# Kernel tuning notes

Measured on AMD Instinct MI355X. Metric: run time of the kernel, lower is better.

The kernel has to match this reference:

```python
import jax, jax.numpy as jnp
import numpy as np

DEPTH = 17                      # tree depth (root at level 0)
D_IN = 128                      # input embedding dim
H = 128                         # hidden dim
N = 2 ** (DEPTH + 1) - 1        # total nodes in complete binary tree, level-major order


def setup_inputs() -> dict:
    key = jax.random.key(0)
    ks = jax.random.split(key, 13)
    s = 0.05
    inp = {"x": jax.random.normal(ks[0], (N, D_IN), jnp.float32)}
    # nn.Linear params; W stored as (in, out) so y = x @ W + b
    gate_names = ["i", "f", "o", "u"]
    for g, k in zip(gate_names, range(1, 5)):
        k1, k2, k3 = jax.random.split(ks[k], 3)
        inp[f"W_{g}"] = jax.random.normal(k1, (D_IN, H), jnp.float32) * s
        inp[f"b_{g}"] = jax.random.normal(k2, (H,), jnp.float32) * s
        inp[f"U_{g}"] = jax.random.normal(k3, (H, H), jnp.float32) * s
    inp["depth"] = DEPTH
    return inp


def reference(x, W_i, b_i, U_i, W_f, b_f, U_f, W_o, b_o, U_o, W_u, b_u, U_u, depth):
    # Precompute input contributions for ALL nodes in one GEMM per gate.
    Xi = x @ W_i + b_i  # [N, H]
    Xf = x @ W_f + b_f
    Xo = x @ W_o + b_o
    Xu = x @ W_u + b_u

    def lvl(l):
        return 2 ** l - 1, 2 ** l  # (start offset, n nodes) at level l

    # Leaves (level = depth): no children -> h_tilde = 0, c = i*u
    s0, n0 = lvl(depth)
    i = jax.nn.sigmoid(Xi[s0:s0 + n0])
    o = jax.nn.sigmoid(Xo[s0:s0 + n0])
    u = jnp.tanh(Xu[s0:s0 + n0])
    c = i * u
    h = o * jnp.tanh(c)

    # Process levels bottom-up; every internal node has exactly 2 children
    for l in range(depth - 1, -1, -1):
        sl, nl = lvl(l)
        ch = h.reshape(nl, 2, H)   # child hidden states per parent
        cc = c.reshape(nl, 2, H)   # child cell states per parent
        h_tilde = ch.sum(axis=1)   # child-sum
        i = jax.nn.sigmoid(Xi[sl:sl + nl] + h_tilde @ U_i)
        o = jax.nn.sigmoid(Xo[sl:sl + nl] + h_tilde @ U_o)
        u = jnp.tanh(Xu[sl:sl + nl] + h_tilde @ U_u)
        # per-child forget gates: f_j = sigmoid(W_f x + U_f h_j)
        f = jax.nn.sigmoid(Xf[sl:sl + nl][:, None, :] + ch @ U_f)  # [nl, 2, H]
        c = i * u + (f * cc).sum(axis=1)
        h = o * jnp.tanh(c)

    # Root (hidden, cell) stacked as [2, H]
    return jnp.stack([h[0], c[0]])
```

## Files before the change

### kernel.cpp

```cpp
#include <hip/hip_runtime.h>
#include <hip/hip_bf16.h>


typedef __bf16 bf16_t;
typedef __bf16 bf16x8 __attribute__((ext_vector_type(8)));
typedef float  f32x4  __attribute__((ext_vector_type(4)));

#define MFMA16(a, b, c) __builtin_amdgcn_mfma_f32_16x16x32_bf16((a), (b), (c), 0, 0, 0)

__device__ __forceinline__ float rcp_(float x) { return __builtin_amdgcn_rcpf(x); }
__device__ __forceinline__ float sigm(float x) { return rcp_(1.0f + __expf(-x)); }
__device__ __forceinline__ float tanh_(float x) {
    float a = fabsf(x);
    float e = __expf(2.0f * a);
    float t = fmaf(-2.0f, rcp_(e + 1.0f), 1.0f);
    return copysignf(t, x);
}

__device__ __forceinline__ void cvt16(const float* __restrict__ src, bf16_t* __restrict__ dst)
{
    float tmp[16];
    *(float4*)&tmp[0]  = ((const float4*)src)[0];
    *(float4*)&tmp[4]  = ((const float4*)src)[1];
    *(float4*)&tmp[8]  = ((const float4*)src)[2];
    *(float4*)&tmp[12] = ((const float4*)src)[3];
    bf16_t b[16];
#pragma unroll
    for (int j = 0; j < 16; j++) b[j] = (bf16_t)tmp[j];
    *(bf16x8*)&dst[0] = *(bf16x8*)&b[0];
    *(bf16x8*)&dst[8] = *(bf16x8*)&b[8];
}

__device__ __forceinline__ void zero16(bf16_t* __restrict__ dst)
{
    bf16x8 z = (bf16x8)(bf16_t)0.f;
    *(bf16x8*)&dst[0] = z;
    *(bf16x8*)&dst[8] = z;
}

__global__ __launch_bounds__(256)
void k_prep(const float* __restrict__ Wi, const float* __restrict__ Wf,
            const float* __restrict__ Wo, const float* __restrict__ Wu,
            const float* __restrict__ Ui, const float* __restrict__ Uf,
            const float* __restrict__ Uo, const float* __restrict__ Uu,
            bf16_t* __restrict__ SW)
{
    int b = blockIdx.x;
    const float* src;
    switch (b) {
        case 0: src = Wi; break; case 1: src = Wf; break;
        case 2: src = Wo; break; case 3: src = Wu; break;
        case 4: src = Ui; break; case 5: src = Uf; break;
        case 6: src = Uo; break; default: src = Uu; break;
    }
    if (b < 4) {
        bf16_t* hi = SW + (size_t)b * 16384;
        for (int idx = threadIdx.x; idx < 16384; idx += 256) {
            int j = idx & 7, ln = (idx >> 3) & 63, kb = (idx >> 9) & 3, nt = idx >> 11;
            int k = kb * 32 + (ln >> 4) * 8 + j;
            int n = nt * 16 + (ln & 15);
            hi[idx] = (bf16_t)src[k * 128 + n];
        }
    } else {
        bf16_t* hi = SW + 65536 + (size_t)(b - 4) * 32768;
        bf16_t* lo = hi + 16384;
        for (int idx = threadIdx.x; idx < 16384; idx += 256) {
            int j = idx & 7, ln = (idx >> 3) & 63, kb = (idx >> 9) & 3, nt = idx >> 11;
            int k = kb * 32 + (ln >> 4) * 8 + j;
            int n = nt * 16 + (ln & 15);
            float w = src[k * 128 + n];
            bf16_t hh = (bf16_t)w;
            hi[idx] = hh;
            lo[idx] = (bf16_t)(w - (float)hh);
        }
    }
}

__device__ __forceinline__ void leaf64(
    const float* __restrict__ x, const bf16_t* __restrict__ SW,
    const float* __restrict__ bi, const float* __restrict__ bo,
    const float* __restrict__ bu,
    bf16_t (* __restrict__ XA)[136],
    bf16_t (* __restrict__ BH)[136], bf16_t (* __restrict__ BC)[136],
    int xRowBase, int tid)
{
    {
        int r = tid >> 3, cb = (tid & 7) * 16;
        cvt16(x + (size_t)(xRowBase + r - 1) * 128 + cb, &XA[r][cb]);
        cvt16(x + (size_t)(xRowBase + r + 31) * 128 + cb, &XA[r + 32][cb]);
    }
    __syncthreads();
    const int wave = tid >> 6, lane = tid & 63;
    const int quad = lane >> 4, lc = lane & 15;

    f32x4 aI[2][4], aO[2][4], aU[2][4];
#pragma unroll
    for (int nt = 0; nt < 2; nt++)
#pragma unroll
        for (int mt = 0; mt < 4; mt++) {
            aI[nt][mt] = (f32x4){0.f, 0.f, 0.f, 0.f};
            aO[nt][mt] = (f32x4){0.f, 0.f, 0.f, 0.f};
            aU[nt][mt] = (f32x4){0.f, 0.f, 0.f, 0.f};
        }
    for (int kb = 0; kb < 4; kb++) {
        const int k0 = kb * 32 + quad * 8;
        bf16x8 a0 = *(const bf16x8*)&XA[lc][k0];
        bf16x8 a1 = *(const bf16x8*)&XA[16 + lc][k0];
        bf16x8 a2 = *(const bf16x8*)&XA[32 + lc][k0];
        bf16x8 a3 = *(const bf16x8*)&XA[48 + lc][k0];
#pragma unroll
        for (int nt = 0; nt < 2; nt++) {
            const size_t boff = ((size_t)((2 * wave + nt) * 4 + kb) * 64 + lane) * 8;
            bf16x8 bWi = *(const bf16x8*)(SW + boff);
            bf16x8 bWo = *(const bf16x8*)(SW + 32768 + boff);
            bf16x8 bWu = *(const bf16x8*)(SW + 49152 + boff);
            aI[nt][0] = MFMA16(a0, bWi, aI[nt][0]);
            aI[nt][1] = MFMA16(a1, bWi, aI[nt][1]);
            aI[nt][2] = MFMA16(a2, bWi, aI[nt][2]);
            aI[nt][3] = MFMA16(a3, bWi, aI[nt][3]);
            aO[nt][0] = MFMA16(a0, bWo, aO[nt][0]);
            aO[nt][1] = MFMA16(a1, bWo, aO[nt][1]);
            aO[nt][2] = MFMA16(a2, bWo, aO[nt][2]);
            aO[nt][3] = MFMA16(a3, bWo, aO[nt][3]);
            aU[nt][0] = MFMA16(a0, bWu, aU[nt][0]);
            aU[nt][1] = MFMA16(a1, bWu, aU[nt][1]);
            aU[nt][2] = MFMA16(a2, bWu, aU[nt][2]);
            aU[nt][3] = MFMA16(a3, bWu, aU[nt][3]);
        }
    }
#pragma unroll
    for (int nt = 0; nt < 2; nt++) {
        const int col = (2 * wave + nt) * 16 + lc;
        float bii = bi[col], boi = bo[col], bui = bu[col];
#pragma unroll
        for (int mt = 0; mt < 4; mt++)
#pragma unroll
            for (int r = 0; r < 4; r++) {
                float iv = sigm(aI[nt][mt][r] + bii);
                float ov = sigm(aO[nt][mt][r] + boi);
                float uv = tanh_(aU[nt][mt][r] + bui);
                float cv = iv * uv;
                int pl = mt * 16 + quad * 4 + r;
                BH[pl][col] = (bf16_t)(ov * tanh_(cv));
                BC[pl][col] = (bf16_t)cv;
            }
    }
    __syncthreads();
}

__device__ __forceinline__ void compute32(
    const float* __restrict__ x, const bf16_t* __restrict__ SW,
    const float* __restrict__ bi, const float* __restrict__ bf_,
    const float* __restrict__ bo, const float* __restrict__ bu,
    bf16_t (* __restrict__ XA)[136], float (* __restrict__ SC)[132],
    const bf16_t (* __restrict__ CH)[136],
    const float* __restrict__ Cglob, int ccBase,
    const bf16_t (* __restrict__ BCc)[136], bool ccLds,
    int xRowBase, int valid,
    bf16_t (* __restrict__ BHo)[136], bf16_t (* __restrict__ BCo)[136], int outRowOff,
    bf16_t* __restrict__ Hg, float* __restrict__ Cg, int outBase,
    bf16_t (* __restrict__ Hd)[136], bool outLds, int tid)
{
    {
        int r = tid >> 3, cb = (tid & 7) * 16;
        if (r < valid) cvt16(x + (size_t)(xRowBase + r - 1) * 128 + cb, &XA[r][cb]);
        else           zero16(&XA[r][cb]);
    }
    __syncthreads();

    const int wave = tid >> 6, lane = tid & 63;
    const int quad = lane >> 4, lc = lane & 15;

    f32x4 aI[2][2], aO[2][2], aU[2][2], aXf[2][2], aF[2][4];
#pragma unroll
    for (int nt = 0; nt < 2; nt++) {
#pragma unroll
        for (int mt = 0; mt < 2; mt++) {
            aI[nt][mt]  = (f32x4){0.f, 0.f, 0.f, 0.f};
            aO[nt][mt]  = (f32x4){0.f, 0.f, 0.f, 0.f};
            aU[nt][mt]  = (f32x4){0.f, 0.f, 0.f, 0.f};
            aXf[nt][mt] = (f32x4){0.f, 0.f, 0.f, 0.f};
        }
#pragma unroll
        for (int mt = 0; mt < 4; mt++) aF[nt][mt] = (f32x4){0.f, 0.f, 0.f, 0.f};
    }

    for (int kb = 0; kb < 4; kb++) {
        const int k0 = kb * 32 + quad * 8;
        bf16x8 xa0 = *(const bf16x8*)&XA[lc][k0];
        bf16x8 xa1 = *(const bf16x8*)&XA[16 + lc][k0];
        bf16x8 h00 = *(const bf16x8*)&CH[2 * lc][k0];
        bf16x8 h01 = *(const bf16x8*)&CH[2 * lc + 1][k0];
        bf16x8 h10 = *(const bf16x8*)&CH[2 * lc + 32][k0];
        bf16x8 h11 = *(const bf16x8*)&CH[2 * lc + 33][k0];
        bf16x8 at0, at1;
#pragma unroll
        for (int j = 0; j < 8; j++) {
            at0[j] = (bf16_t)((float)h00[j] + (float)h01[j]);
            at1[j] = (bf16_t)((float)h10[j] + (float)h11[j]);
        }
        bf16x8 ac0 = *(const bf16x8*)&CH[lc][k0];
        bf16x8 ac1 = *(const bf16x8*)&CH[16 + lc][k0];
        bf16x8 ac2 = *(const bf16x8*)&CH[32 + lc][k0];
        bf16x8 ac3 = *(const bf16x8*)&CH[48 + lc][k0];
#pragma unroll
        for (int nt = 0; nt < 2; nt++) {
            const size_t boff = ((size_t)((2 * wave + nt) * 4 + kb) * 64 + lane) * 8;
            bf16x8 bWi = *(const bf16x8*)(SW + boff);
            bf16x8 bWf = *(const bf16x8*)(SW + 16384 + boff);
            bf16x8 bWo = *(const bf16x8*)(SW + 32768 + boff);
            bf16x8 bWu = *(const bf16x8*)(SW + 49152 + boff);
            aI[nt][0]  = MFMA16(xa0, bWi, aI[nt][0]);
            aI[nt][1]  = MFMA16(xa1, bWi, aI[nt][1]);
            aXf[nt][0] = MFMA16(xa0, bWf, aXf[nt][0]);
            aXf[nt][1] = MFMA16(xa1, bWf, aXf[nt][1]);
            aO[nt][0]  = MFMA16(xa0, bWo, aO[nt][0]);
            aO[nt][1]  = MFMA16(xa1, bWo, aO[nt][1]);
            aU[nt][0]  = MFMA16(xa0, bWu, aU[nt][0]);
            aU[nt][1]  = MFMA16(xa1, bWu, aU[nt][1]);
            const bf16_t* Ub = SW + 65536;
            bf16x8 bIh = *(const bf16x8*)(Ub + boff);
            bf16x8 bIl = *(const bf16x8*)(Ub + 16384 + boff);
            aI[nt][0] = MFMA16(at0, bIh, aI[nt][0]);
            aI[nt][0] = MFMA16(at0, bIl, aI[nt][0]);
            aI[nt][1] = MFMA16(at1, bIh, aI[nt][1]);
            aI[nt][1] = MFMA16(at1, bIl, aI[nt][1]);
            bf16x8 bOh = *(const bf16x8*)(Ub + 65536 + boff);
            bf16x8 bOl = *(const bf16x8*)(Ub + 81920 + boff);
            aO[nt][0] = MFMA16(at0, bOh, aO[nt][0]);
            aO[nt][0] = MFMA16(at0, bOl, aO[nt][0]);
            aO[nt][1] = MFMA16(at1, bOh, aO[nt][1]);
            aO[nt][1] = MFMA16(at1, bOl, aO[nt][1]);
            bf16x8 bUh = *(const bf16x8*)(Ub + 98304 + boff);
            bf16x8 bUl = *(const bf16x8*)(Ub + 114688 + boff);
            aU[nt][0] = MFMA16(at0, bUh, aU[nt][0]);
            aU[nt][0] = MFMA16(at0, bUl, aU[nt][0]);
            aU[nt][1] = MFMA16(at1, bUh, aU[nt][1]);
            aU[nt][1] = MFMA16(at1, bUl, aU[nt][1]);
            bf16x8 bFh = *(const bf16x8*)(Ub + 32768 + boff);
            bf16x8 bFl = *(const bf16x8*)(Ub + 49152 + boff);
            aF[nt][0] = MFMA16(ac0, bFh, aF[nt][0]);
            aF[nt][0] = MFMA16(ac0, bFl, aF[nt][0]);
            aF[nt][1] = MFMA16(ac1, bFh, aF[nt][1]);
            aF[nt][1] = MFMA16(ac1, bFl, aF[nt][1]);
            aF[nt][2] = MFMA16(ac2, bFh, aF[nt][2]);
            aF[nt][2] = MFMA16(ac2, bFl, aF[nt][2]);
            aF[nt][3] = MFMA16(ac3, bFh, aF[nt][3]);
            aF[nt][3] = MFMA16(ac3, bFl, aF[nt][3]);
        }
    }
    __syncthreads();

#pragma unroll
    for (int nt = 0; nt < 2; nt++) {
        const int col = (2 * wave + nt) * 16 + lc;
        float bfv = bf_[col];
#pragma unroll
        for (int mt = 0; mt < 2; mt++)
#pragma unroll
            for (int r = 0; r < 4; r++)
                SC[mt * 16 + quad * 4 + r][col] = aXf[nt][mt][r] + bfv;
    }
    __syncthreads();

    float Sv[2][4][2];
#pragma unroll
    for (int nt = 0; nt < 2; nt++) {
        const int col = (2 * wave + nt) * 16 + lc;
#pragma unroll
        for (int mt = 0; mt < 4; mt++)
#pragma unroll
            for (int pi = 0; pi < 2; pi++) {
                int pl = mt * 8 + quad * 2 + pi;
                float xf = SC[pl][col];
                float f0 = sigm(xf + aF[nt][mt][2 * pi]);
                float f1 = sigm(xf + aF[nt][mt][2 * pi + 1]);
                float c0, c1;
                if (ccLds) {
                    c0 = (float)BCc[2 * pl][col];
                    c1 = (float)BCc[2 * pl + 1][col];
                } else {
                    size_t cr = (size_t)(ccBase + 2 * pl) * 128 + col;
                    c0 = Cglob[cr];
                    c1 = Cglob[cr + 128];
                }
                Sv[nt][mt][pi] = f0 * c0 + f1 * c1;
            }
    }
    __syncthreads();
#pragma unroll
    for (int nt = 0; nt < 2; nt++) {
        const int col = (2 * wave + nt) * 16 + lc;
#pragma unroll
        for (int mt = 0; mt < 4; mt++)
#pragma unroll
            for (int pi = 0; pi < 2; pi++)
                SC[mt * 8 + quad * 2 + pi][col] = Sv[nt][mt][pi];
    }
    __syncthreads();

    float hr[2][2][4];
#pragma unroll
    for (int nt = 0; nt < 2; nt++) {
        const int col = (2 * wave + nt) * 16 + lc;
        float bii = bi[col], boi = bo[col], bui = bu[col];
#pragma unroll
        for (int mt = 0; mt < 2; mt++)
#pragma unroll
            for (int r = 0; r < 4; r++) {
                int pl = mt * 16 + quad * 4 + r;
                float iv = sigm(aI[nt][mt][r] + bii);
                float ov = sigm(aO[nt][mt][r] + boi);
                float uv = tanh_(aU[nt][mt][r] + bui);
                float cv = iv * uv + SC[pl][col];
                float hv = ov * tanh_(cv);
                hr[nt][mt][r] = hv;
                if (outLds) {
                    BHo[outRowOff + pl][col] = (bf16_t)hv;
                    BCo[outRowOff + pl][col] = (bf16_t)cv;
                } else if (pl < valid) {
                    Cg[(size_t)(outBase + pl) * 128 + col] = cv;
                }
            }
    }
    if (outLds) {
        __syncthreads();
    } else {
        __syncthreads();
#pragma unroll
        for (int nt = 0; nt < 2; nt++) {
            const int col = (2 * wave + nt) * 16 + lc;
#pragma unroll
            for (int mt = 0; mt < 2; mt++)
#pragma unroll
                for (int r = 0; r < 4; r++)
                    Hd[mt * 16 + quad * 4 + r][col] = (bf16_t)hr[nt][mt][r];
        }
        __syncthreads();
        int r = tid >> 3, cb = (tid & 7) * 16;
        if (r < valid) {
            uint4* dst = (uint4*)(Hg + (size_t)(outBase + r) * 128 + cb);
            dst[0] = *(uint4*)&Hd[r][cb];
            dst[1] = *(uint4*)&Hd[r][cb + 8];
        }
        __syncthreads();
    }
}

__global__ __launch_bounds__(256)
void k_pairleaf(const float* __restrict__ x, const bf16_t* __restrict__ SW,
                const float* __restrict__ bi, const float* __restrict__ bf_,
                const float* __restrict__ bo, const float* __restrict__ bu,
                bf16_t* __restrict__ H, float* __restrict__ C, int Pa)
{
    __shared__ __align__(16) char smem[52224];
    bf16_t (*XA)[136] = (bf16_t(*)[136])(smem);
    float  (*SC)[132] = (float(*)[132])(smem);
    bf16_t (*Hd)[136] = (bf16_t(*)[136])(smem + 8704);
    bf16_t (*BH)[136] = (bf16_t(*)[136])(smem + 17408);
    bf16_t (*BC)[136] = (bf16_t(*)[136])(smem + 34816);

    const int tid = threadIdx.x;
    const int sA0 = Pa + 32 * blockIdx.x;

    leaf64(x, SW, bi, bo, bu, XA, BH, BC, 2 * sA0, tid);

    compute32(x, SW, bi, bf_, bo, bu, XA, SC,
              (const bf16_t(*)[136])BH,
              nullptr, 0, (const bf16_t(*)[136])BC, true,
              sA0, 32,
              nullptr, nullptr, 0,
              H, C, sA0, Hd, false, tid);
}

__global__ __launch_bounds__(256)
void k_pair(const float* __restrict__ x, const bf16_t* __restrict__ SW,
            const float* __restrict__ bi, const float* __restrict__ bf_,
            const float* __restrict__ bo, const float* __restrict__ bu,
            bf16_t* __restrict__ H, float* __restrict__ C,
            int Pa)
{
    __shared__ __align__(16) char smem[60928];
    bf16_t (*XA)[136] = (bf16_t(*)[136])(smem);
    bf16_t (*HC)[136] = (bf16_t(*)[136])(smem + 8704);
    float  (*SC)[132] = (float(*)[132])(smem);
    bf16_t (*BH)[136] = (bf16_t(*)[136])(smem + 26112);
    bf16_t (*BC)[136] = (bf16_t(*)[136])(smem + 43520);

    const int tid = threadIdx.x;
    const int t   = blockIdx.x;
    const int sA0 = Pa + 32 * t;
    int Pta = Pa - 32 * t; if (Pta > 32) Pta = 32;

    if (Pta < 32) {
        bf16x8 z = (bf16x8)(bf16_t)0.f;
        for (int i = tid; i < 64 * 17; i += 256) {
            ((bf16x8*)BH)[i] = z;
            ((bf16x8*)BC)[i] = z;
        }
    }

    for (int q = 0; q < 2; q++) {
        int bvalid = 2 * Pa - (64 * t + 32 * q);
        if (bvalid > 32) bvalid = 32;
        if (bvalid <= 0) break;
        {
            int r = tid >> 2, cb = (tid & 3) * 32;
            if (r < 2 * bvalid) {
                const uint4* src = (const uint4*)(H + (size_t)(4 * sA0 + 64 * q + r) * 128 + cb);
                *(uint4*)&HC[r][cb]      = src[0];
                *(uint4*)&HC[r][cb + 8]  = src[1];
                *(uint4*)&HC[r][cb + 16] = src[2];
                *(uint4*)&HC[r][cb + 24] = src[3];
            } else {
                uint4 z = {0u, 0u, 0u, 0u};
                *(uint4*)&HC[r][cb]      = z;
                *(uint4*)&HC[r][cb + 8]  = z;
                *(uint4*)&HC[r][cb + 16] = z;
                *(uint4*)&HC[r][cb + 24] = z;
            }
        }
        compute32(x, SW, bi, bf_, bo, bu, XA, SC,
                  (const bf16_t(*)[136])HC,
                  C, 4 * sA0 + 64 * q, nullptr, false,
                  2 * sA0 + 32 * q, bvalid,
                  BH, BC, 32 * q,
                  nullptr, nullptr, 0, nullptr, true, tid);
    }

    compute32(x, SW, bi, bf_, bo, bu, XA, SC,
              (const bf16_t(*)[136])BH,
              nullptr, 0, (const bf16_t(*)[136])BC, true,
              sA0, Pta,
              nullptr, nullptr, 0,
              H, C, sA0, HC, false, tid);
}

__global__ __launch_bounds__(256, 2)
void k_lvl(const float* __restrict__ x, const bf16_t* __restrict__ SW,
           const float* __restrict__ bi, const float* __restrict__ bf_,
           const float* __restrict__ bo, const float* __restrict__ bu,
           bf16_t* H, float* C, int np)
{
    __shared__ __align__(16) char smem[75264];
    f32x4  (*PR)[4][64] = (f32x4(*)[4][64])smem;
    bf16_t (*XA)[136]   = (bf16_t(*)[136])(smem + 49152);
    bf16_t (*CH)[136]   = (bf16_t(*)[136])(smem + 57856);
    float  (*SC)[17]    = (float(*)[17])smem;

    const int tid = threadIdx.x;
    const int wave = tid >> 6, lane = tid & 63;
    const int quad = lane >> 4, lc = lane & 15;

    const int task = blockIdx.x;
    const int ct = task & 7, mt = task >> 3;
    int valid = np - 32 * mt; if (valid > 32) valid = 32;
    if (valid <= 0) return;
    const int prow = np + 32 * mt;
    const int crow = 2 * np + 64 * mt;

    {
        int r = tid >> 3, cb = (tid & 7) * 16;
        if (r < valid) cvt16(x + (size_t)(prow - 1 + r) * 128 + cb, &XA[r][cb]);
        else           zero16(&XA[r][cb]);
    }
    {
        int r = tid >> 2, cb = (tid & 3) * 32;
        if (r < 2 * valid) {
            const uint4* src = (const uint4*)(H + (size_t)(crow + r) * 128 + cb);
            *(uint4*)&CH[r][cb]      = src[0];
            *(uint4*)&CH[r][cb + 8]  = src[1];
            *(uint4*)&CH[r][cb + 16] = src[2];
            *(uint4*)&CH[r][cb + 24] = src[3];
        } else {
            uint4 z = {0u, 0u, 0u, 0u};
            *(uint4*)&CH[r][cb]      = z;
            *(uint4*)&CH[r][cb + 8]  = z;
            *(uint4*)&CH[r][cb + 16] = z;
            *(uint4*)&CH[r][cb + 24] = z;
        }
    }
    __syncthreads();

    f32x4 z4 = (f32x4){0.f, 0.f, 0.f, 0.f};
    f32x4 aI0 = z4, aI1 = z4, aXf0 = z4, aXf1 = z4;
    f32x4 aO0 = z4, aO1 = z4, aU0 = z4, aU1 = z4;
    f32x4 aF0 = z4, aF1 = z4, aF2 = z4, aF3 = z4;
    {
        const int k0 = wave * 32 + quad * 8;
        bf16x8 xa0 = *(const bf16x8*)&XA[lc][k0];
        bf16x8 xa1 = *(const bf16x8*)&XA[16 + lc][k0];
        bf16x8 h00 = *(const bf16x8*)&CH[2 * lc][k0];
        bf16x8 h01 = *(const bf16x8*)&CH[2 * lc + 1][k0];
        bf16x8 h10 = *(const bf16x8*)&CH[2 * lc + 32][k0];
        bf16x8 h11 = *(const bf16x8*)&CH[2 * lc + 33][k0];
        bf16x8 at0, at1;
#pragma unroll
        for (int j = 0; j < 8; j++) {
            at0[j] = (bf16_t)((float)h00[j] + (float)h01[j]);
            at1[j] = (bf16_t)((float)h10[j] + (float)h11[j]);
        }
        bf16x8 ac0 = *(const bf16x8*)&CH[lc][k0];
        bf16x8 ac1 = *(const bf16x8*)&CH[16 + lc][k0];
        bf16x8 ac2 = *(const bf16x8*)&CH[32 + lc][k0];
        bf16x8 ac3 = *(const bf16x8*)&CH[48 + lc][k0];

        const size_t boff = ((size_t)(ct * 4 + wave) * 64 + lane) * 8;
        bf16x8 bWi = *(const bf16x8*)(SW + boff);
        bf16x8 bWf = *(const bf16x8*)(SW + 16384 + boff);
        bf16x8 bWo = *(const bf16x8*)(SW + 32768 + boff);
        bf16x8 bWu = *(const bf16x8*)(SW + 49152 + boff);
        const bf16_t* Ub = SW + 65536;
        bf16x8 bIh = *(const bf16x8*)(Ub + boff);
        bf16x8 bIl = *(const bf16x8*)(Ub + 16384 + boff);
        bf16x8 bFh = *(const bf16x8*)(Ub + 32768 + boff);
        bf16x8 bFl = *(const bf16x8*)(Ub + 49152 + boff);
        bf16x8 bOh = *(const bf16x8*)(Ub + 65536 + boff);
        bf16x8 bOl = *(const bf16x8*)(Ub + 81920 + boff);
        bf16x8 bUh = *(const bf16x8*)(Ub + 98304 + boff);
        bf16x8 bUl = *(const bf16x8*)(Ub + 114688 + boff);

        aI0  = MFMA16(xa0, bWi, aI0);  aI1  = MFMA16(xa1, bWi, aI1);
        aXf0 = MFMA16(xa0, bWf, aXf0); aXf1 = MFMA16(xa1, bWf, aXf1);
        aO0  = MFMA16(xa0, bWo, aO0);  aO1  = MFMA16(xa1, bWo, aO1);
        aU0  = MFMA16(xa0, bWu, aU0);  aU1  = MFMA16(xa1, bWu, aU1);
        aI0 = MFMA16(at0, bIh, aI0); aI0 = MFMA16(at0, bIl, aI0);
        aI1 = MFMA16(at1, bIh, aI1); aI1 = MFMA16(at1, bIl, aI1);
        aO0 = MFMA16(at0, bOh, aO0); aO0 = MFMA16(at0, bOl, aO0);
        aO1 = MFMA16(at1, bOh, aO1); aO1 = MFMA16(at1, bOl, aO1);
        aU0 = MFMA16(at0, bUh, aU0); aU0 = MFMA16(at0, bUl, aU0);
        aU1 = MFMA16(at1, bUh, aU1); aU1 = MFMA16(at1, bUl, aU1);
        aF0 = MFMA16(ac0, bFh, aF0); aF0 = MFMA16(ac0, bFl, aF0);
        aF1 = MFMA16(ac1, bFh, aF1); aF1 = MFMA16(ac1, bFl, aF1);
        aF2 = MFMA16(ac2, bFh, aF2); aF2 = MFMA16(ac2, bFl, aF2);
        aF3 = MFMA16(ac3, bFh, aF3); aF3 = MFMA16(ac3, bFl, aF3);
    }
    if (wave != 0) {
        PR[0][wave][lane]  = aI0;  PR[1][wave][lane]  = aI1;
        PR[2][wave][lane]  = aXf0; PR[3][wave][lane]  = aXf1;
        PR[4][wave][lane]  = aO0;  PR[5][wave][lane]  = aO1;
        PR[6][wave][lane]  = aU0;  PR[7][wave][lane]  = aU1;
        PR[8][wave][lane]  = aF0;  PR[9][wave][lane]  = aF1;
        PR[10][wave][lane] = aF2;  PR[11][wave][lane] = aF3;
    }
    __syncthreads();
    if (wave == 0) {
        aI0  += PR[0][1][lane]  + PR[0][2][lane]  + PR[0][3][lane];
        aI1  += PR[1][1][lane]  + PR[1][2][lane]  + PR[1][3][lane];
        aXf0 += PR[2][1][lane]  + PR[2][2][lane]  + PR[2][3][lane];
        aXf1 += PR[3][1][lane]  + PR[3][2][lane]  + PR[3][3][lane];
        aO0  += PR[4][1][lane]  + PR[4][2][lane]  + PR[4][3][lane];
        aO1  += PR[5][1][lane]  + PR[5][2][lane]  + PR[5][3][lane];
        aU0  += PR[6][1][lane]  + PR[6][2][lane]  + PR[6][3][lane];
        aU1  += PR[7][1][lane]  + PR[7][2][lane]  + PR[7][3][lane];
        aF0  += PR[8][1][lane]  + PR[8][2][lane]  + PR[8][3][lane];
        aF1  += PR[9][1][lane]  + PR[9][2][lane]  + PR[9][3][lane];
        aF2  += PR[10][1][lane] + PR[10][2][lane] + PR[10][3][lane];
        aF3  += PR[11][1][lane] + PR[11][2][lane] + PR[11][3][lane];

        const int colg = ct * 16 + lc;
        float c0v[4][2], c1v[4][2];
#pragma unroll
        for (int m2 = 0; m2 < 4; m2++)
#pragma unroll
            for (int pi = 0; pi < 2; pi++) {
                int pl = m2 * 8 + quad * 2 + pi;
                size_t cr = (size_t)(crow + 2 * pl) * 128 + colg;
                c0v[m2][pi] = C[cr];
                c1v[m2][pi] = C[cr + 128];
            }
        float bfv = bf_[colg];
#pragma unroll
        for (int r = 0; r < 4; r++) {
            SC[quad * 4 + r][lc]      = aXf0[r] + bfv;
            SC[16 + quad * 4 + r][lc] = aXf1[r] + bfv;
        }
#define NS_FPATH(M2, AF)                                            \
        _Pragma("unroll")                                           \
        for (int pi = 0; pi < 2; pi++) {                            \
            int pl = M2 * 8 + quad * 2 + pi;                        \
            float xf = SC[pl][lc];                                  \
            float f0 = sigm(xf + AF[2 * pi]);                       \
            float f1 = sigm(xf + AF[2 * pi + 1]);                   \
            SC[pl][lc] = f0 * c0v[M2][pi] + f1 * c1v[M2][pi];       \
        }
        NS_FPATH(0, aF0) NS_FPATH(1, aF1) NS_FPATH(2, aF2) NS_FPATH(3, aF3)
#undef NS_FPATH
        float bii = bi[colg], boi = bo[colg], bui = bu[colg];
#define NS_IOU(MT, AI, AO, AU)                                      \
        _Pragma("unroll")                                           \
        for (int r = 0; r < 4; r++) {                               \
            int pl = MT * 16 + quad * 4 + r;                        \
            float iv = sigm(AI[r] + bii);                           \
            float ov = sigm(AO[r] + boi);                           \
            float uv = tanh_(AU[r] + bui);                          \
            float cv = iv * uv + SC[pl][lc];                        \
            if (pl < valid) {                                       \
                H[(size_t)(prow + pl) * 128 + colg] = (bf16_t)(ov * tanh_(cv)); \
                C[(size_t)(prow + pl) * 128 + colg] = cv;           \
            }                                                       \
        }
        NS_IOU(0, aI0, aO0, aU0)
        NS_IOU(1, aI1, aO1, aU1)
#undef NS_IOU
    }
}

__global__ __launch_bounds__(256)
void k_out(const bf16_t* __restrict__ H, const float* __restrict__ C,
           float* __restrict__ out)
{
    int t = threadIdx.x;
    if (t < 128)      out[t] = (float)H[128 + t];
    else if (t < 256) out[t] = C[t];
}

extern "C" void kernel_launch(void* const* d_in, const int* in_sizes, int n_in,
                              void* d_out, int out_size, void* d_ws, size_t ws_size,
                              hipStream_t stream)
{
    const float* x   = (const float*)d_in[0];
    const float* Wi  = (const float*)d_in[1];
    const float* bi  = (const float*)d_in[2];
    const float* Ui  = (const float*)d_in[3];
    const float* Wf  = (const float*)d_in[4];
    const float* bf_ = (const float*)d_in[5];
    const float* Uf  = (const float*)d_in[6];
    const float* Wo  = (const float*)d_in[7];
    const float* bo  = (const float*)d_in[8];
    const float* Uo  = (const float*)d_in[9];
    const float* Wu  = (const float*)d_in[10];
    const float* bu  = (const float*)d_in[11];
    const float* Uu  = (const float*)d_in[12];

    int Ntot  = in_sizes[0] / 128;
    int depth = 31 - __builtin_clz((unsigned)(Ntot + 1)) - 1;

    char* w = (char*)d_ws;
    bf16_t* SW = (bf16_t*)w;  w += 393216;
    bf16_t* H  = (bf16_t*)w;  w += (size_t)(Ntot + 1) * 128 * sizeof(bf16_t);
    float*  C  = (float*)w;

    k_prep<<<8, 256, 0, stream>>>(Wi, Wf, Wo, Wu, Ui, Uf, Uo, Uu, SW);

    {
        int Pa = 1 << (depth - 1);
        k_pairleaf<<<Pa / 32, 256, 0, stream>>>(x, SW, bi, bf_, bo, bu, H, C, Pa);
    }
    int lowest = depth - 1;
    for (int A = depth - 3; A >= 14; A -= 2) {
        int Pa = 1 << A;
        int blocks = (Pa + 31) / 32;
        k_pair<<<blocks, 256, 0, stream>>>(x, SW, bi, bf_, bo, bu, H, C, Pa);
        lowest = A;
    }
    for (int l = lowest - 1; l >= 0; l--) {
        int np = 1 << l;
        int nmt = (np + 31) / 32;
        k_lvl<<<nmt * 8, 256, 0, stream>>>(x, SW, bi, bf_, bo, bu, H, C, np);
    }
    k_out<<<1, 256, 0, stream>>>(H, C, (float*)d_out);
}
```

Baseline: 514.8 us.

## Rewrite leaf-pair kernel with 512 threads, one wave per column tile

The fused leaf-plus-parent kernel now launches 512 threads, and each of its 8 waves owns one 16-column output tile instead of two. A new per-wave node routine computes all gates for the 32 parents, using a small per-wave scratch buffer for the forget path. It writes H and C straight to global memory rather than staging through shared memory with extra barriers. This is meant to raise parallelism and cut register pressure and synchronisation in the largest level. In exchange it uses more shared memory per block (68 KB) and makes uncoalesced column-strided global stores.

```diff
diff --git a/kernel.cpp b/kernel.cpp
--- a/kernel.cpp
+++ b/kernel.cpp
@@ -76,76 +76,203 @@
     }
 }
 
-__device__ __forceinline__ void leaf64(
-    const float* __restrict__ x, const bf16_t* __restrict__ SW,
+__device__ __forceinline__ void node32_wave(
+    const bf16_t* __restrict__ SW,
+    const float* __restrict__ bi, const float* __restrict__ bf_,
+    const float* __restrict__ bo, const float* __restrict__ bu,
+    const bf16_t (* __restrict__ XA)[136],
+    const bf16_t (* __restrict__ CH)[136],
+    const bf16_t (* __restrict__ BCc)[136],
+    float (* __restrict__ SCw)[17],
+    int ct,
+    bf16_t* __restrict__ Hg, float* __restrict__ Cg, int outBase,
+    int lane)
+{
+    const int quad = lane >> 4, lc = lane & 15;
+    f32x4 z4 = (f32x4){0.f, 0.f, 0.f, 0.f};
+    f32x4 aI0 = z4, aI1 = z4, aXf0 = z4, aXf1 = z4;
+    f32x4 aO0 = z4, aO1 = z4, aU0 = z4, aU1 = z4;
+    f32x4 aF0 = z4, aF1 = z4, aF2 = z4, aF3 = z4;
+
+#pragma unroll
+    for (int kb = 0; kb < 4; kb++) {
+        const int k0 = kb * 32 + quad * 8;
+        bf16x8 xa0 = *(const bf16x8*)&XA[lc][k0];
+        bf16x8 xa1 = *(const bf16x8*)&XA[16 + lc][k0];
+        bf16x8 h00 = *(const bf16x8*)&CH[2 * lc][k0];
+        bf16x8 h01 = *(const bf16x8*)&CH[2 * lc + 1][k0];
+        bf16x8 h10 = *(const bf16x8*)&CH[2 * lc + 32][k0];
+        bf16x8 h11 = *(const bf16x8*)&CH[2 * lc + 33][k0];
+        bf16x8 at0, at1;
+#pragma unroll
+        for (int j = 0; j < 8; j++) {
+            at0[j] = (bf16_t)((float)h00[j] + (float)h01[j]);
+            at1[j] = (bf16_t)((float)h10[j] + (float)h11[j]);
+        }
+        bf16x8 ac0 = *(const bf16x8*)&CH[lc][k0];
+        bf16x8 ac1 = *(const bf16x8*)&CH[16 + lc][k0];
+        bf16x8 ac2 = *(const bf16x8*)&CH[32 + lc][k0];
+        bf16x8 ac3 = *(const bf16x8*)&CH[48 + lc][k0];
+
+        const size_t boff = ((size_t)(ct * 4 + kb) * 64 + lane) * 8;
+        bf16x8 bWi = *(const bf16x8*)(SW + boff);
+        bf16x8 bWf = *(const bf16x8*)(SW + 16384 + boff);
+        bf16x8 bWo = *(const bf16x8*)(SW + 32768 + boff);
+        bf16x8 bWu = *(const bf16x8*)(SW + 49152 + boff);
+        const bf16_t* Ub = SW + 65536;
+        bf16x8 bIh = *(const bf16x8*)(Ub + boff);
+        bf16x8 bIl = *(const bf16x8*)(Ub + 16384 + boff);
+        bf16x8 bFh = *(const bf16x8*)(Ub + 32768 + boff);
+        bf16x8 bFl = *(const bf16x8*)(Ub + 49152 + boff);
+        bf16x8 bOh = *(const bf16x8*)(Ub + 65536 + boff);
+        bf16x8 bOl = *(const bf16x8*)(Ub + 81920 + boff);
+        bf16x8 bUh = *(const bf16x8*)(Ub + 98304 + boff);
+        bf16x8 bUl = *(const bf16x8*)(Ub + 114688 + boff);
+
+        aI0  = MFMA16(xa0, bWi, aI0);  aI1  = MFMA16(xa1, bWi, aI1);
+        aXf0 = MFMA16(xa0, bWf, aXf0); aXf1 = MFMA16(xa1, bWf, aXf1);
+        aO0  = MFMA16(xa0, bWo, aO0);  aO1  = MFMA16(xa1, bWo, aO1);
+        aU0  = MFMA16(xa0, bWu, aU0);  aU1  = MFMA16(xa1, bWu, aU1);
+        aI0 = MFMA16(at0, bIh, aI0); aI0 = MFMA16(at0, bIl, aI0);
+        aI1 = MFMA16(at1, bIh, aI1); aI1 = MFMA16(at1, bIl, aI1);
+        aO0 = MFMA16(at0, bOh, aO0); aO0 = MFMA16(at0, bOl, aO0);
+        aO1 = MFMA16(at1, bOh, aO1); aO1 = MFMA16(at1, bOl, aO1);
+        aU0 = MFMA16(at0, bUh, aU0); aU0 = MFMA16(at0, bUl, aU0);
+        aU1 = MFMA16(at1, bUh, aU1); aU1 = MFMA16(at1, bUl, aU1);
+        aF0 = MFMA16(ac0, bFh, aF0); aF0 = MFMA16(ac0, bFl, aF0);
+        aF1 = MFMA16(ac1, bFh, aF1); aF1 = MFMA16(ac1, bFl, aF1);
+        aF2 = MFMA16(ac2, bFh, aF2); aF2 = MFMA16(ac2, bFl, aF2);
+        aF3 = MFMA16(ac3, bFh, aF3); aF3 = MFMA16(ac3, bFl, aF3);
+    }
+
+    const int colg = ct * 16 + lc;
+    float c0v[4][2], c1v[4][2];
+#pragma unroll
+    for (int m2 = 0; m2 < 4; m2++)
+#pragma unroll
+        for (int pi = 0; pi < 2; pi++) {
+            int pl = m2 * 8 + quad * 2 + pi;
+            c0v[m2][pi] = (float)BCc[2 * pl][colg];
+            c1v[m2][pi] = (float)BCc[2 * pl + 1][colg];
+        }
+    float bfv = bf_[colg];
+#pragma unroll
+    for (int r = 0; r < 4; r++) {
+        SCw[quad * 4 + r][lc]      = aXf0[r] + bfv;
+        SCw[16 + quad * 4 + r][lc] = aXf1[r] + bfv;
+    }
+#define NS_FPATH(M2, AF)                                            \
+    _Pragma("unroll")                                               \
+    for (int pi = 0; pi < 2; pi++) {                                \
+        int pl = M2 * 8 + quad * 2 + pi;                            \
+        float xf = SCw[pl][lc];                                     \
+        float f0 = sigm(xf + AF[2 * pi]);                           \
+        float f1 = sigm(xf + AF[2 * pi + 1]);                       \
+        SCw[pl][lc] = f0 * c0v[M2][pi] + f1 * c1v[M2][pi];          \
+    }
+    NS_FPATH(0, aF0) NS_FPATH(1, aF1) NS_FPATH(2, aF2) NS_FPATH(3, aF3)
+#undef NS_FPATH
+    float bii = bi[colg], boi = bo[colg], bui = bu[colg];
+#define NS_IOU(MT, AI, AO, AU)                                      \
+    _Pragma("unroll")                                               \
+    for (int r = 0; r < 4; r++) {                                   \
+        int pl = MT * 16 + quad * 4 + r;                            \
+        float iv = sigm(AI[r] + bii);                               \
+        float ov = sigm(AO[r] + boi);                               \
+        float uv = tanh_(AU[r] + bui);                              \
+        float cv = iv * uv + SCw[pl][lc];                           \
+        float hv = ov * tanh_(cv);                                  \
+        Hg[(size_t)(outBase + pl) * 128 + colg] = (bf16_t)hv;       \
+        Cg[(size_t)(outBase + pl) * 128 + colg] = cv;               \
+    }
+    NS_IOU(0, aI0, aO0, aU0)
+    NS_IOU(1, aI1, aO1, aU1)
+#undef NS_IOU
+}
+
+__device__ __forceinline__ void leaf64_wave(
+    const bf16_t* __restrict__ SW,
     const float* __restrict__ bi, const float* __restrict__ bo,
     const float* __restrict__ bu,
-    bf16_t (* __restrict__ XA)[136],
+    const bf16_t (* __restrict__ XA)[136],
     bf16_t (* __restrict__ BH)[136], bf16_t (* __restrict__ BC)[136],
-    int xRowBase, int tid)
-{
-    {
-        int r = tid >> 3, cb = (tid & 7) * 16;
-        cvt16(x + (size_t)(xRowBase + r - 1) * 128 + cb, &XA[r][cb]);
-        cvt16(x + (size_t)(xRowBase + r + 31) * 128 + cb, &XA[r + 32][cb]);
-    }
-    __syncthreads();
-    const int wave = tid >> 6, lane = tid & 63;
+    int ct, int lane)
+{
     const int quad = lane >> 4, lc = lane & 15;
-
-    f32x4 aI[2][4], aO[2][4], aU[2][4];
-#pragma unroll
-    for (int nt = 0; nt < 2; nt++)
-#pragma unroll
-        for (int mt = 0; mt < 4; mt++) {
-            aI[nt][mt] = (f32x4){0.f, 0.f, 0.f, 0.f};
-            aO[nt][mt] = (f32x4){0.f, 0.f, 0.f, 0.f};
-            aU[nt][mt] = (f32x4){0.f, 0.f, 0.f, 0.f};
-        }
+    f32x4 aI[4], aO[4], aU[4];
+#pragma unroll
+    for (int mt = 0; mt < 4; mt++) {
+        aI[mt] = (f32x4){0.f, 0.f, 0.f, 0.f};
+        aO[mt] = (f32x4){0.f, 0.f, 0.f, 0.f};
+        aU[mt] = (f32x4){0.f, 0.f, 0.f, 0.f};
+    }
+#pragma unroll
     for (int kb = 0; kb < 4; kb++) {
         const int k0 = kb * 32 + quad * 8;
         bf16x8 a0 = *(const bf16x8*)&XA[lc][k0];
         bf16x8 a1 = *(const bf16x8*)&XA[16 + lc][k0];
         bf16x8 a2 = *(const bf16x8*)&XA[32 + lc][k0];
         bf16x8 a3 = *(const bf16x8*)&XA[48 + lc][k0];
-#pragma unroll
-        for (int nt = 0; nt < 2; nt++) {
-            const size_t boff = ((size_t)((2 * wave + nt) * 4 + kb) * 64 + lane) * 8;
-            bf16x8 bWi = *(const bf16x8*)(SW + boff);
-            bf16x8 bWo = *(const bf16x8*)(SW + 32768 + boff);
-            bf16x8 bWu = *(const bf16x8*)(SW + 49152 + boff);
-            aI[nt][0] = MFMA16(a0, bWi, aI[nt][0]);
-            aI[nt][1] = MFMA16(a1, bWi, aI[nt][1]);
-            aI[nt][2] = MFMA16(a2, bWi, aI[nt][2]);
-            aI[nt][3] = MFMA16(a3, bWi, aI[nt][3]);
-            aO[nt][0] = MFMA16(a0, bWo, aO[nt][0]);
-            aO[nt][1] = MFMA16(a1, bWo, aO[nt][1]);
-            aO[nt][2] = MFMA16(a2, bWo, aO[nt][2]);
-            aO[nt][3] = MFMA16(a3, bWo, aO[nt][3]);
-            aU[nt][0] = MFMA16(a0, bWu, aU[nt][0]);
-            aU[nt][1] = MFMA16(a1, bWu, aU[nt][1]);
-            aU[nt][2] = MFMA16(a2, bWu, aU[nt][2]);
-            aU[nt][3] = MFMA16(a3, bWu, aU[nt][3]);
-        }
-    }
-#pragma unroll
-    for (int nt = 0; nt < 2; nt++) {
-        const int col = (2 * wave + nt) * 16 + lc;
-        float bii = bi[col], boi = bo[col], bui = bu[col];
-#pragma unroll
-        for (int mt = 0; mt < 4; mt++)
-#pragma unroll
-            for (int r = 0; r < 4; r++) {
-                float iv = sigm(aI[nt][mt][r] + bii);
-                float ov = sigm(aO[nt][mt][r] + boi);
-                float uv = tanh_(aU[nt][mt][r] + bui);
-                float cv = iv * uv;
-                int pl = mt * 16 + quad * 4 + r;
-                BH[pl][col] = (bf16_t)(ov * tanh_(cv));
-                BC[pl][col] = (bf16_t)cv;
-            }
-    }
-    __syncthreads();
+        const size_t boff = ((size_t)(ct * 4 + kb) * 64 + lane) * 8;
+        bf16x8 bWi = *(const bf16x8*)(SW + boff);
+        bf16x8 bWo = *(const bf16x8*)(SW + 32768 + boff);
+        bf16x8 bWu = *(const bf16x8*)(SW + 49152 + boff);
+        aI[0] = MFMA16(a0, bWi, aI[0]); aI[1] = MFMA16(a1, bWi, aI[1]);
+        aI[2] = MFMA16(a2, bWi, aI[2]); aI[3] = MFMA16(a3, bWi, aI[3]);
+        aO[0] = MFMA16(a0, bWo, aO[0]); aO[1] = MFMA16(a1, bWo, aO[1]);
+        aO[2] = MFMA16(a2, bWo, aO[2]); aO[3] = MFMA16(a3, bWo, aO[3]);
+        aU[0] = MFMA16(a0, bWu, aU[0]); aU[1] = MFMA16(a1, bWu, aU[1]);
+        aU[2] = MFMA16(a2, bWu, aU[2]); aU[3] = MFMA16(a3, bWu, aU[3]);
+    }
+    const int col = ct * 16 + lc;
+    float bii = bi[col], boi = bo[col], bui = bu[col];
+#pragma unroll
+    for (int mt = 0; mt < 4; mt++)
+#pragma unroll
+        for (int r = 0; r < 4; r++) {
+            float iv = sigm(aI[mt][r] + bii);
+            float ov = sigm(aO[mt][r] + boi);
+            float uv = tanh_(aU[mt][r] + bui);
+            float cv = iv * uv;
+            int pl = mt * 16 + quad * 4 + r;
+            BH[pl][col] = (bf16_t)(ov * tanh_(cv));
+            BC[pl][col] = (bf16_t)cv;
+        }
+}
+
+__global__ __launch_bounds__(512)
+void k_pairleaf2(const float* __restrict__ x, const bf16_t* __restrict__ SW,
+                 const float* __restrict__ bi, const float* __restrict__ bf_,
+                 const float* __restrict__ bo, const float* __restrict__ bu,
+                 bf16_t* __restrict__ H, float* __restrict__ C, int Pa)
+{
+    __shared__ __align__(16) char smem[69632];
+    bf16_t (*XA)[136] = (bf16_t(*)[136])(smem);
+    bf16_t (*BH)[136] = (bf16_t(*)[136])(smem + 17408);
+    bf16_t (*BC)[136] = (bf16_t(*)[136])(smem + 34816);
+    float  (*SC)[32][17] = (float(*)[32][17])(smem + 52224);
+
+    const int tid = threadIdx.x;
+    const int wave = tid >> 6, lane = tid & 63;
+    const int sA0 = Pa + 32 * blockIdx.x;
+
+    {
+        int r = tid >> 3, cb = (tid & 7) * 16;
+        cvt16(x + (size_t)(2 * sA0 - 1 + r) * 128 + cb, &XA[r][cb]);
+    }
+    __syncthreads();
+    leaf64_wave(SW, bi, bo, bu, (const bf16_t(*)[136])XA, BH, BC, wave, lane);
+    __syncthreads();
+    {
+        int r = tid >> 3, cb = (tid & 7) * 16;
+        if (r < 32) cvt16(x + (size_t)(sA0 - 1 + r) * 128 + cb, &XA[r][cb]);
+    }
+    __syncthreads();
+    node32_wave(SW, bi, bf_, bo, bu,
+                (const bf16_t(*)[136])XA, (const bf16_t(*)[136])BH,
+                (const bf16_t(*)[136])BC,
+                SC[wave], wave,
+                H, C, sA0, lane);
 }
 
 __device__ __forceinline__ void compute32(
@@ -348,32 +475,6 @@
 }
 
 __global__ __launch_bounds__(256)
-void k_pairleaf(const float* __restrict__ x, const bf16_t* __restrict__ SW,
-                const float* __restrict__ bi, const float* __restrict__ bf_,
-                const float* __restrict__ bo, const float* __restrict__ bu,
-                bf16_t* __restrict__ H, float* __restrict__ C, int Pa)
-{
-    __shared__ __align__(16) char smem[52224];
-    bf16_t (*XA)[136] = (bf16_t(*)[136])(smem);
-    float  (*SC)[132] = (float(*)[132])(smem);
-    bf16_t (*Hd)[136] = (bf16_t(*)[136])(smem + 8704);
-    bf16_t (*BH)[136] = (bf16_t(*)[136])(smem + 17408);
-    bf16_t (*BC)[136] = (bf16_t(*)[136])(smem + 34816);
-
-    const int tid = threadIdx.x;
-    const int sA0 = Pa + 32 * blockIdx.x;
-
-    leaf64(x, SW, bi, bo, bu, XA, BH, BC, 2 * sA0, tid);
-
-    compute32(x, SW, bi, bf_, bo, bu, XA, SC,
-              (const bf16_t(*)[136])BH,
-              nullptr, 0, (const bf16_t(*)[136])BC, true,
-              sA0, 32,
-              nullptr, nullptr, 0,
-              H, C, sA0, Hd, false, tid);
-}
-
-__global__ __launch_bounds__(256)
 void k_pair(const float* __restrict__ x, const bf16_t* __restrict__ SW,
             const float* __restrict__ bi, const float* __restrict__ bf_,
             const float* __restrict__ bo, const float* __restrict__ bu,
@@ -645,7 +746,7 @@
 
     {
         int Pa = 1 << (depth - 1);
-        k_pairleaf<<<Pa / 32, 256, 0, stream>>>(x, SW, bi, bf_, bo, bu, H, C, Pa);
+        k_pairleaf2<<<Pa / 32, 512, 0, stream>>>(x, SW, bi, bf_, bo, bu, H, C, Pa);
     }
     int lowest = depth - 1;
     for (int A = depth - 3; A >= 14; A -= 2) {
```

New measurement: 470.8 us. -8.6%, faster.
